# Kernel tuning notes

Measured on AMD Instinct MI355X. Metric: run time of the kernel, lower is better.

Reference implementation:

```python
import jax, jax.numpy as jnp
import numpy as np
from jax import lax

B, S, F, C = 64, 2048, 256, 32


def setup_inputs() -> dict:
    key = jax.random.key(0)
    ks = jax.random.split(key, 6)
    return {
        "X": jax.random.normal(ks[0], (B, S, F), dtype=jnp.float32),
        "W": jax.random.normal(ks[1], (C, F), dtype=jnp.float32) * (1.0 / np.sqrt(F)),
        "b": jax.random.normal(ks[2], (C,), dtype=jnp.float32) * 0.01,
        "transitions": jax.random.normal(ks[3], (C, C), dtype=jnp.float32) * 0.1,
        "start_transitions": jax.random.normal(ks[4], (C,), dtype=jnp.float32) * 0.1,
        "end_transitions": jax.random.normal(ks[5], (C,), dtype=jnp.float32) * 0.1,
    }


def reference(X, W, b, transitions, start_transitions, end_transitions):
    # Affine projection to emission scores: [B, S, C]
    emissions = jnp.einsum("bsf,cf->bsc", X, W) + b
    e = jnp.moveaxis(emissions, 1, 0)  # [S, B, C] for scan over time

    alpha0 = start_transitions[None, :] + e[0]  # [B, C]

    def viterbi_step(alpha, e_t):
        # scores[b, i, j] = alpha[b, i] + T[i, j] + e_t[b, j]
        scores = alpha[:, :, None] + transitions[None, :, :] + e_t[:, None, :]
        best = jnp.max(scores, axis=1)      # [B, C]
        bp = jnp.argmax(scores, axis=1)     # [B, C] backpointers
        return best, bp

    alpha_T, backptrs = lax.scan(viterbi_step, alpha0, e[1:])  # backptrs: [S-1, B, C]

    final = alpha_T + end_transitions[None, :]
    best_score = jnp.max(final, axis=-1)              # [B]
    last_tag = jnp.argmax(final, axis=-1)             # [B]

    def backtrack(tag, bp):
        prev = jnp.take_along_axis(bp, tag[:, None], axis=1)[:, 0]
        return prev, prev

    _, prev_tags = lax.scan(backtrack, last_tag, backptrs, reverse=True)  # [S-1, B]
    path = jnp.concatenate([prev_tags, last_tag[None, :]], axis=0)        # [S, B]
    return best_score, jnp.moveaxis(path, 0, 1)  # ([B], [B, S])
```

## Files before the change

### kernel.cpp

```cpp
#include <hip/hip_runtime.h>

#define BB 64
#define SS 2048
#define FF 256
#define CC 32
#define CH 64

typedef unsigned u32x2 __attribute__((ext_vector_type(2)));

__device__ __forceinline__ void plswap16(int a_in, int& x, int& y) {
#if __has_builtin(__builtin_amdgcn_permlane16_swap)
    u32x2 r = __builtin_amdgcn_permlane16_swap((unsigned)a_in, (unsigned)a_in, false, false);
    x = (int)r[0]; y = (int)r[1];
#else
    int xx = a_in, yy;
    asm volatile("v_mov_b32 %0, %1" : "=v"(yy) : "v"(a_in));
    asm volatile("v_permlane16_swap_b32 %0, %1" : "+v"(xx), "+v"(yy));
    x = xx; y = yy;
#endif
}
__device__ __forceinline__ void plswap32(int a_in, int& x, int& y) {
#if __has_builtin(__builtin_amdgcn_permlane32_swap)
    u32x2 r = __builtin_amdgcn_permlane32_swap((unsigned)a_in, (unsigned)a_in, false, false);
    x = (int)r[0]; y = (int)r[1];
#else
    int xx = a_in, yy;
    asm volatile("v_mov_b32 %0, %1" : "=v"(yy) : "v"(a_in));
    asm volatile("v_permlane32_swap_b32 %0, %1" : "+v"(xx), "+v"(yy));
    x = xx; y = yy;
#endif
}

#if __has_builtin(__builtin_amdgcn_mov_dpp)
#define ROT1(d, s, K) d = __builtin_amdgcn_mov_dpp(s, 0x120 + K, 0xF, 0xF, false)
#else
#define ROT1(d, s, K) d = __builtin_amdgcn_update_dpp(s, s, 0x120 + K, 0xF, 0xF, false)
#endif
#define ROTALL(arr, s) \
    arr[0] = s;        \
    ROT1(arr[1], s, 1);  ROT1(arr[2], s, 2);  ROT1(arr[3], s, 3);  \
    ROT1(arr[4], s, 4);  ROT1(arr[5], s, 5);  ROT1(arr[6], s, 6);  \
    ROT1(arr[7], s, 7);  ROT1(arr[8], s, 8);  ROT1(arr[9], s, 9);  \
    ROT1(arr[10], s, 10); ROT1(arr[11], s, 11); ROT1(arr[12], s, 12); \
    ROT1(arr[13], s, 13); ROT1(arr[14], s, 14); ROT1(arr[15], s, 15)

__device__ __forceinline__ float fmax3_(float a, float b, float c) { return fmaxf(fmaxf(a, b), c); }

__global__ __launch_bounds__(256) void emis_kernel(const float* __restrict__ X,
                                                   const float* __restrict__ W,
                                                   const float* __restrict__ bias,
                                                   float* __restrict__ em) {
    __shared__ __align__(16) float wsh[32 * 260];
    const int tid = threadIdx.x;
    const long rowbase = (long)blockIdx.x * 64;

    const float4* Wg = (const float4*)W;
#pragma unroll
    for (int i = 0; i < 8; ++i) {
        int idx = tid + i * 256;
        int r = idx >> 6, c4 = idx & 63;
        *(float4*)&wsh[r * 260 + c4 * 4] = Wg[idx];
    }
    __syncthreads();

    const int rp = tid >> 3;
    const int cgp = tid & 7;
    const long r0 = rowbase + 2 * rp, r1 = r0 + 1;
    const float4* X0 = (const float4*)(X + r0 * FF);
    const float4* X1 = (const float4*)(X + r1 * FF);

    float acc0[4] = {0.f, 0.f, 0.f, 0.f};
    float acc1[4] = {0.f, 0.f, 0.f, 0.f};

#pragma unroll 8
    for (int k4 = 0; k4 < 64; ++k4) {
        float4 xa = X0[k4];
        float4 xb = X1[k4];
#pragma unroll
        for (int jj = 0; jj < 4; ++jj) {
            float4 w = *(const float4*)&wsh[(cgp + 8 * jj) * 260 + k4 * 4];
            acc0[jj] = fmaf(xa.x, w.x, acc0[jj]);
            acc0[jj] = fmaf(xa.y, w.y, acc0[jj]);
            acc0[jj] = fmaf(xa.z, w.z, acc0[jj]);
            acc0[jj] = fmaf(xa.w, w.w, acc0[jj]);
            acc1[jj] = fmaf(xb.x, w.x, acc1[jj]);
            acc1[jj] = fmaf(xb.y, w.y, acc1[jj]);
            acc1[jj] = fmaf(xb.z, w.z, acc1[jj]);
            acc1[jj] = fmaf(xb.w, w.w, acc1[jj]);
        }
    }
#pragma unroll
    for (int jj = 0; jj < 4; ++jj) {
        int c = cgp + 8 * jj;
        float bj = bias[c];
        em[r0 * CC + c] = acc0[jj] + bj;
        em[r1 * CC + c] = acc1[jj] + bj;
    }
}

#define STEP2_ASM(avar, evar)                                                       \
    do {                                                                            \
        float x_, b_, q0_, q1_, q2_, q3_, q4_, q5_, q6_, q7_,                       \
              q8_, q9_, q10_, q11_, q12_, q13_, q14_, q15_;                         \
        asm volatile(                                                               \
            "v_mov_b32 %[x], %[aa]\n\t"                                             \
            "s_nop 1\n\t"                                                           \
            "v_permlane16_swap_b32 %[x], %[aa]\n\t"                                 \
            "s_nop 0\n\t"                                                           \
            "v_cndmask_b32 %[bb], %[aa], %[x], %[m16]\n\t"                          \
            "s_nop 1\n\t"                                                           \
            "v_add_f32 %[q0], %[bb], %[t0]\n\t"                                     \
            "v_add_f32_dpp %[q1], %[bb], %[t1] row_ror:1 row_mask:0xf bank_mask:0xf\n\t"  \
            "v_add_f32_dpp %[q2], %[bb], %[t2] row_ror:2 row_mask:0xf bank_mask:0xf\n\t"  \
            "v_add_f32_dpp %[q3], %[bb], %[t3] row_ror:3 row_mask:0xf bank_mask:0xf\n\t"  \
            "v_add_f32_dpp %[q4], %[bb], %[t4] row_ror:4 row_mask:0xf bank_mask:0xf\n\t"  \
            "v_add_f32_dpp %[q5], %[bb], %[t5] row_ror:5 row_mask:0xf bank_mask:0xf\n\t"  \
            "v_add_f32_dpp %[q6], %[bb], %[t6] row_ror:6 row_mask:0xf bank_mask:0xf\n\t"  \
            "v_add_f32_dpp %[q7], %[bb], %[t7] row_ror:7 row_mask:0xf bank_mask:0xf\n\t"  \
            "v_add_f32_dpp %[q8], %[bb], %[t8] row_ror:8 row_mask:0xf bank_mask:0xf\n\t"  \
            "v_add_f32_dpp %[q9], %[bb], %[t9] row_ror:9 row_mask:0xf bank_mask:0xf\n\t"  \
            "v_add_f32_dpp %[q10], %[bb], %[t10] row_ror:10 row_mask:0xf bank_mask:0xf\n\t" \
            "v_add_f32_dpp %[q11], %[bb], %[t11] row_ror:11 row_mask:0xf bank_mask:0xf\n\t" \
            "v_add_f32_dpp %[q12], %[bb], %[t12] row_ror:12 row_mask:0xf bank_mask:0xf\n\t" \
            "v_add_f32_dpp %[q13], %[bb], %[t13] row_ror:13 row_mask:0xf bank_mask:0xf\n\t" \
            "v_add_f32_dpp %[q14], %[bb], %[t14] row_ror:14 row_mask:0xf bank_mask:0xf\n\t" \
            "v_add_f32_dpp %[q15], %[bb], %[t15] row_ror:15 row_mask:0xf bank_mask:0xf\n\t" \
            "v_max3_f32 %[q0], %[q0], %[q1], %[q2]\n\t"                             \
            "v_max3_f32 %[q3], %[q3], %[q4], %[q5]\n\t"                             \
            "v_max3_f32 %[q6], %[q6], %[q7], %[q8]\n\t"                             \
            "v_max3_f32 %[q9], %[q9], %[q10], %[q11]\n\t"                           \
            "v_max3_f32 %[q12], %[q12], %[q13], %[q14]\n\t"                         \
            "v_max3_f32 %[q0], %[q0], %[q3], %[q6]\n\t"                             \
            "v_max3_f32 %[q9], %[q9], %[q12], %[q15]\n\t"                           \
            "v_max_f32 %[q0], %[q0], %[q9]\n\t"                                     \
            "v_mov_b32 %[x], %[q0]\n\t"                                             \
            "s_nop 1\n\t"                                                           \
            "v_permlane32_swap_b32 %[x], %[q0]\n\t"                                 \
            "s_nop 0\n\t"                                                           \
            "v_max_f32 %[q0], %[q0], %[x]\n\t"                                      \
            "v_add_f32 %[aa], %[q0], %[ee]\n\t"                                     \
            : [aa] "+v"(avar), [x] "=&v"(x_), [bb] "=&v"(b_),                       \
              [q0] "=&v"(q0_), [q1] "=&v"(q1_), [q2] "=&v"(q2_), [q3] "=&v"(q3_),   \
              [q4] "=&v"(q4_), [q5] "=&v"(q5_), [q6] "=&v"(q6_), [q7] "=&v"(q7_),   \
              [q8] "=&v"(q8_), [q9] "=&v"(q9_), [q10] "=&v"(q10_),                  \
              [q11] "=&v"(q11_), [q12] "=&v"(q12_), [q13] "=&v"(q13_),              \
              [q14] "=&v"(q14_), [q15] "=&v"(q15_)                                  \
            : [ee] "v"(evar), [t0] "v"(Ti[0]), [t1] "v"(Ti[1]), [t2] "v"(Ti[2]),    \
              [t3] "v"(Ti[3]), [t4] "v"(Ti[4]), [t5] "v"(Ti[5]), [t6] "v"(Ti[6]),   \
              [t7] "v"(Ti[7]), [t8] "v"(Ti[8]), [t9] "v"(Ti[9]), [t10] "v"(Ti[10]), \
              [t11] "v"(Ti[11]), [t12] "v"(Ti[12]), [t13] "v"(Ti[13]),              \
              [t14] "v"(Ti[14]), [t15] "v"(Ti[15]),                                 \
              [m16] "s"(mask16));                                                   \
    } while (0)

__global__ __launch_bounds__(64, 1) void viterbi_fwd4(float* __restrict__ em,
                                                      const float* __restrict__ T,
                                                      const float* __restrict__ startT,
                                                      const float* __restrict__ endT,
                                                      float* __restrict__ out) {
    const int l = threadIdx.x;
    const int b = blockIdx.x;
    const int j = l & 31;
    const int h = l >> 5;

    int p0, p1;
    plswap16(j, p0, p1);
    const bool c16 = (((p0 >> 4) & 1) == h);
    const int pm = c16 ? p0 : p1;
    int mk[16];
    ROTALL(mk, pm);

    const unsigned long long mask16 = __ballot(c16);

    float Ti[16];
#pragma unroll
    for (int k = 0; k < 16; ++k) Ti[k] = T[mk[k] * CC + j];

    float* eb = em + (long)b * SS * CC;

    float eq[8];
#pragma unroll
    for (int v = 0; v < 8; ++v) eq[v] = eb[v * 32 + j];

    float a = startT[j] + eq[0];
    eb[j] = a;
    eq[0] = eb[8 * 32 + j];

    int t = 1;
    for (int g = 0; g < 254; ++g) {
#pragma unroll
        for (int u = 0; u < 8; ++u) {
            STEP2_ASM(a, eq[t & 7]);
            eb[t * 32 + j] = a;
            eq[t & 7] = eb[(t + 8) * 32 + j];
            ++t;
        }
    }
#pragma unroll
    for (int u = 0; u < 7; ++u) {
        STEP2_ASM(a, eq[t & 7]);
        eb[t * 32 + j] = a;
        eq[t & 7] = eb[(t + 8) * 32 + j];
        ++t;
    }
#pragma unroll
    for (int u = 0; u < 8; ++u) {
        STEP2_ASM(a, eq[t & 7]);
        eb[t * 32 + j] = a;
        ++t;
    }

    float v = a + endT[j];
    int idx = j;
#pragma unroll
    for (int d = 1; d <= 16; d <<= 1) {
        float ovv = __shfl_xor(v, d);
        int   oii = __shfl_xor(idx, d);
        bool c = (ovv > v) || (ovv == v && oii < idx);
        v = c ? ovv : v;
        idx = c ? oii : idx;
    }
    if (l == 0) {
        out[b] = v;
        out[BB + (long)b * SS + (SS - 1)] = (float)idx;
    }
}

__global__ __launch_bounds__(64, 2) void bp_compose(const float* __restrict__ alpha,
                                                    const float* __restrict__ T,
                                                    unsigned* __restrict__ bp,
                                                    unsigned char* __restrict__ G) {
    const int l = threadIdx.x;
    const int j = l & 31;
    const int h = l >> 5;
    const int b = blockIdx.x >> 6;
    const int k = blockIdx.x & 63;

    int p0, p1;
    plswap16(j, p0, p1);
    const bool c16 = (((p0 >> 4) & 1) == h);
    const int pm = c16 ? p0 : p1;
    int mk[16];
    ROTALL(mk, pm);
    int q0p, q1p;
    plswap32(l, q0p, q1p);
    const bool pick0 = (q0p == (l ^ 32));

    float Ti[16];
    unsigned Bk[16];
#pragma unroll
    for (int kk = 0; kk < 16; ++kk) {
        Ti[kk] = T[mk[kk] * CC + j];
        Bk[kk] = 1u << mk[kk];
    }

    const float* A = alpha + (long)b * SS * CC;
    const int u0 = k << 5;

    float aq[8];
#pragma unroll
    for (int v = 0; v < 8; ++v) aq[v] = A[(u0 + v) * CC + j];

    unsigned sr[8];
#pragma unroll
    for (int p = 0; p < 8; ++p) sr[p] = 0u;

#pragma unroll
    for (int g8 = 0; g8 < 4; ++g8) {
#pragma unroll
        for (int v = 0; v < 8; ++v) {
            const int u = g8 * 8 + v;
            float av = aq[v];
            if (g8 < 3) aq[v] = A[(u0 + (g8 + 1) * 8 + v) * CC + j];

            int x, y;
            plswap16(__float_as_int(av), x, y);
            int base = c16 ? x : y;
            int rot[16];
            ROTALL(rot, base);
            float s[16];
#pragma unroll
            for (int kk = 0; kk < 16; ++kk) s[kk] = __int_as_float(rot[kk]) + Ti[kk];

            float m0 = fmax3_(s[0], s[1], s[2]);
            float m1 = fmax3_(s[3], s[4], s[5]);
            float m2 = fmax3_(s[6], s[7], s[8]);
            float m3 = fmax3_(s[9], s[10], s[11]);
            float m4 = fmax3_(s[12], s[13], s[14]);
            float mv = fmaxf(fmax3_(m0, m1, m2), fmax3_(m3, m4, s[15]));

            int xm, ym;
            plswap32(__float_as_int(mv), xm, ym);
            float ov = __int_as_float(pick0 ? xm : ym);
            float gv = fmaxf(mv, ov);

            unsigned c0 = (s[0] == gv) ? Bk[0] : 0u,   c1 = (s[1] == gv) ? Bk[1] : 0u;
            unsigned c2 = (s[2] == gv) ? Bk[2] : 0u,   c3 = (s[3] == gv) ? Bk[3] : 0u;
            unsigned c4 = (s[4] == gv) ? Bk[4] : 0u,   c5 = (s[5] == gv) ? Bk[5] : 0u;
            unsigned c6 = (s[6] == gv) ? Bk[6] : 0u,   c7 = (s[7] == gv) ? Bk[7] : 0u;
            unsigned c8 = (s[8] == gv) ? Bk[8] : 0u,   c9 = (s[9] == gv) ? Bk[9] : 0u;
            unsigned c10 = (s[10] == gv) ? Bk[10] : 0u, c11 = (s[11] == gv) ? Bk[11] : 0u;
            unsigned c12 = (s[12] == gv) ? Bk[12] : 0u, c13 = (s[13] == gv) ? Bk[13] : 0u;
            unsigned c14 = (s[14] == gv) ? Bk[14] : 0u, c15 = (s[15] == gv) ? Bk[15] : 0u;
            unsigned msk = ((c0 | c1 | c2) | (c3 | c4 | c5)) |
                           ((c6 | c7 | c8) | (c9 | c10 | c11)) |
                           ((c12 | c13 | c14) | c15);

            int xk, yk;
            plswap32((int)msk, xk, yk);
            unsigned om = (unsigned)(pick0 ? xk : yk);
            int wi = __builtin_ctz(msk | om);

            if (u == 31 && k == CH - 1) wi = j;
            sr[u >> 2] |= (unsigned)wi << ((u & 3) * 8);
        }
    }

#pragma unroll
    for (int p = 0; p < 8; ++p)
        bp[((unsigned)(8 * k + p) * BB + b) * CC + j] = sr[p];

    int g = j;
#pragma unroll
    for (int rel = 31; rel >= 0; --rel) {
        unsigned dw = (unsigned)__builtin_amdgcn_ds_bpermute((g | (l & 32)) << 2,
                                                             (int)sr[rel >> 2]);
        g = (int)((dw >> ((rel & 3) * 8)) & 31u);
    }
    G[(b * CH + k) * 32 + j] = (unsigned char)g;
}

__global__ __launch_bounds__(64) void bt_scan(const unsigned char* __restrict__ G,
                                              const float* __restrict__ out,
                                              int* __restrict__ tagB) {
    __shared__ unsigned char Gs[32 * CH * 32];
    const int l = threadIdx.x;
    const int bbase = blockIdx.x * 32;
    const float4* Gg = (const float4*)(G + (size_t)bbase * CH * 32);
    float4* Gls = (float4*)Gs;
#pragma unroll
    for (int i = 0; i < 64; ++i) Gls[l + i * 64] = Gg[l + i * 64];
    __syncthreads();

    if (l < 32) {
        const int b = bbase + l;
        int cur = (int)out[BB + (long)b * SS + (SS - 1)];
        for (int k = CH - 1; k >= 0; --k) {
            cur = Gs[(l * CH + k) * 32 + cur];
            tagB[b * CH + k] = cur;
        }
    }
}

__global__ __launch_bounds__(64, 4) void bt_emit(const unsigned* __restrict__ bp,
                                                 const int* __restrict__ tagB,
                                                 const float* __restrict__ outR,
                                                 float* __restrict__ out) {
    const int l = threadIdx.x;
    const int b = blockIdx.x >> 6;
    const int k = blockIdx.x & 63;

    unsigned sr[8];
#pragma unroll
    for (int p = 0; p < 8; ++p) sr[p] = bp[((unsigned)(8 * k + p) * BB + b) * CC + (l & 31)];

    int start = (k == CH - 1) ? (int)outR[BB + (long)b * SS + (SS - 1)]
                              : tagB[b * CH + k + 1];
    int g = start, cap = start;
#pragma unroll
    for (int rel = 31; rel >= 0; --rel) {
        unsigned dw = (unsigned)__builtin_amdgcn_ds_bpermute((g | (l & 32)) << 2,
                                                             (int)sr[rel >> 2]);
        g = (int)((dw >> ((rel & 3) * 8)) & 31u);
        cap = (l == rel) ? g : cap;
    }
    if (l < 32) out[BB + (long)b * SS + k * 32 + l] = (float)cap;
}

extern "C" void kernel_launch(void* const* d_in, const int* in_sizes, int n_in,
                              void* d_out, int out_size, void* d_ws, size_t ws_size,
                              hipStream_t stream) {
    const float* X      = (const float*)d_in[0];
    const float* W      = (const float*)d_in[1];
    const float* bias   = (const float*)d_in[2];
    const float* T      = (const float*)d_in[3];
    const float* startT = (const float*)d_in[4];
    const float* endT   = (const float*)d_in[5];
    float* out = (float*)d_out;

    float*    em = (float*)d_ws;
    unsigned* bp = (unsigned*)((char*)d_ws + (size_t)BB * SS * CC * 4);
    unsigned char* G    = (unsigned char*)d_ws + (20u << 20);
    int*           tagB = (int*)((char*)d_ws + (20u << 20) + 131072);

    emis_kernel<<<(BB * SS) / 64, 256, 0, stream>>>(X, W, bias, em);
    viterbi_fwd4<<<BB, 64, 0, stream>>>(em, T, startT, endT, out);
    bp_compose<<<BB * CH, 64, 0, stream>>>(em, T, bp, G);
    bt_scan<<<2, 64, 0, stream>>>(G, out, tagB);
    bt_emit<<<BB * CH, 64, 0, stream>>>(bp, tagB, out, out);
}
```

Measured before the change: 260.2 us.

## Fuse emission GEMM with Viterbi forward via per-batch progress counters

Merges the emission projection and the forward Viterbi recurrence into one launch. Emission blocks publish completion through per-batch atomic counters, and the forward wavefronts poll those counters so the serial recurrence can start while the remaining emissions are still being computed. Alpha values are now packed four timesteps per float4 store, and bp_compose reads them back in that matching packed layout. This relies on emission blocks being scheduled before the spinning forward blocks, and it adds a memset plus polling overhead.

```diff
diff --git a/kernel.cpp b/kernel.cpp
--- a/kernel.cpp
+++ b/kernel.cpp
@@ -45,58 +45,6 @@
     ROT1(arr[13], s, 13); ROT1(arr[14], s, 14); ROT1(arr[15], s, 15)
 
 __device__ __forceinline__ float fmax3_(float a, float b, float c) { return fmaxf(fmaxf(a, b), c); }
-
-__global__ __launch_bounds__(256) void emis_kernel(const float* __restrict__ X,
-                                                   const float* __restrict__ W,
-                                                   const float* __restrict__ bias,
-                                                   float* __restrict__ em) {
-    __shared__ __align__(16) float wsh[32 * 260];
-    const int tid = threadIdx.x;
-    const long rowbase = (long)blockIdx.x * 64;
-
-    const float4* Wg = (const float4*)W;
-#pragma unroll
-    for (int i = 0; i < 8; ++i) {
-        int idx = tid + i * 256;
-        int r = idx >> 6, c4 = idx & 63;
-        *(float4*)&wsh[r * 260 + c4 * 4] = Wg[idx];
-    }
-    __syncthreads();
-
-    const int rp = tid >> 3;
-    const int cgp = tid & 7;
-    const long r0 = rowbase + 2 * rp, r1 = r0 + 1;
-    const float4* X0 = (const float4*)(X + r0 * FF);
-    const float4* X1 = (const float4*)(X + r1 * FF);
-
-    float acc0[4] = {0.f, 0.f, 0.f, 0.f};
-    float acc1[4] = {0.f, 0.f, 0.f, 0.f};
-
-#pragma unroll 8
-    for (int k4 = 0; k4 < 64; ++k4) {
-        float4 xa = X0[k4];
-        float4 xb = X1[k4];
-#pragma unroll
-        for (int jj = 0; jj < 4; ++jj) {
-            float4 w = *(const float4*)&wsh[(cgp + 8 * jj) * 260 + k4 * 4];
-            acc0[jj] = fmaf(xa.x, w.x, acc0[jj]);
-            acc0[jj] = fmaf(xa.y, w.y, acc0[jj]);
-            acc0[jj] = fmaf(xa.z, w.z, acc0[jj]);
-            acc0[jj] = fmaf(xa.w, w.w, acc0[jj]);
-            acc1[jj] = fmaf(xb.x, w.x, acc1[jj]);
-            acc1[jj] = fmaf(xb.y, w.y, acc1[jj]);
-            acc1[jj] = fmaf(xb.z, w.z, acc1[jj]);
-            acc1[jj] = fmaf(xb.w, w.w, acc1[jj]);
-        }
-    }
-#pragma unroll
-    for (int jj = 0; jj < 4; ++jj) {
-        int c = cgp + 8 * jj;
-        float bj = bias[c];
-        em[r0 * CC + c] = acc0[jj] + bj;
-        em[r1 * CC + c] = acc1[jj] + bj;
-    }
-}
 
 #define STEP2_ASM(avar, evar)                                                       \
     do {                                                                            \
@@ -153,13 +101,76 @@
               [m16] "s"(mask16));                                                   \
     } while (0)
 
-__global__ __launch_bounds__(64, 1) void viterbi_fwd4(float* __restrict__ em,
+__global__ __launch_bounds__(256) void fused_emis_fwd(const float* __restrict__ X,
+                                                      const float* __restrict__ W,
+                                                      const float* __restrict__ bias,
                                                       const float* __restrict__ T,
                                                       const float* __restrict__ startT,
                                                       const float* __restrict__ endT,
-                                                      float* __restrict__ out) {
+                                                      float* __restrict__ em,
+                                                      float* __restrict__ out,
+                                                      int* __restrict__ prog) {
+    __shared__ __align__(16) float wsh[32 * 260];
+
+    if (blockIdx.x < 2048) {
+        const int tid = threadIdx.x;
+        const int g = blockIdx.x >> 6;
+        const int b = blockIdx.x & 63;
+        const long rowbase = (long)b * SS + (long)g * 64;
+
+        const float4* Wg = (const float4*)W;
+#pragma unroll
+        for (int i = 0; i < 8; ++i) {
+            int idx = tid + i * 256;
+            int r = idx >> 6, c4 = idx & 63;
+            *(float4*)&wsh[r * 260 + c4 * 4] = Wg[idx];
+        }
+        __syncthreads();
+
+        const int rp = tid >> 3;
+        const int cgp = tid & 7;
+        const long r0 = rowbase + 2 * rp, r1 = r0 + 1;
+        const float4* X0 = (const float4*)(X + r0 * FF);
+        const float4* X1 = (const float4*)(X + r1 * FF);
+
+        float acc0[4] = {0.f, 0.f, 0.f, 0.f};
+        float acc1[4] = {0.f, 0.f, 0.f, 0.f};
+
+#pragma unroll 8
+        for (int k4 = 0; k4 < 64; ++k4) {
+            float4 xa = X0[k4];
+            float4 xb = X1[k4];
+#pragma unroll
+            for (int jj = 0; jj < 4; ++jj) {
+                float4 w = *(const float4*)&wsh[(cgp + 8 * jj) * 260 + k4 * 4];
+                acc0[jj] = fmaf(xa.x, w.x, acc0[jj]);
+                acc0[jj] = fmaf(xa.y, w.y, acc0[jj]);
+                acc0[jj] = fmaf(xa.z, w.z, acc0[jj]);
+                acc0[jj] = fmaf(xa.w, w.w, acc0[jj]);
+                acc1[jj] = fmaf(xb.x, w.x, acc1[jj]);
+                acc1[jj] = fmaf(xb.y, w.y, acc1[jj]);
+                acc1[jj] = fmaf(xb.z, w.z, acc1[jj]);
+                acc1[jj] = fmaf(xb.w, w.w, acc1[jj]);
+            }
+        }
+#pragma unroll
+        for (int jj = 0; jj < 4; ++jj) {
+            int c = cgp + 8 * jj;
+            float bj = bias[c];
+            em[r0 * CC + c] = acc0[jj] + bj;
+            em[r1 * CC + c] = acc1[jj] + bj;
+        }
+
+        __syncthreads();
+        __threadfence();
+        if (tid == 0)
+            __hip_atomic_fetch_add(&prog[b], 1, __ATOMIC_RELEASE, __HIP_MEMORY_SCOPE_AGENT);
+        return;
+    }
+
+    if (threadIdx.x >= 64) return;
     const int l = threadIdx.x;
-    const int b = blockIdx.x;
+    const int b = blockIdx.x - 2048;
     const int j = l & 31;
     const int h = l >> 5;
 
@@ -176,39 +187,60 @@
 #pragma unroll
     for (int k = 0; k < 16; ++k) Ti[k] = T[mk[k] * CC + j];
 
+    int* pb = prog + b;
+    auto pollb = [&](int need) {
+        while (__hip_atomic_load(pb, __ATOMIC_ACQUIRE, __HIP_MEMORY_SCOPE_AGENT) < need)
+            __builtin_amdgcn_s_sleep(2);
+    };
+
     float* eb = em + (long)b * SS * CC;
+    float4* ev4 = (float4*)eb;
+
+    pollb(2);
 
     float eq[8];
 #pragma unroll
     for (int v = 0; v < 8; ++v) eq[v] = eb[v * 32 + j];
 
+    float4 av;
     float a = startT[j] + eq[0];
-    eb[j] = a;
+    av.x = a;
     eq[0] = eb[8 * 32 + j];
 
     int t = 1;
     for (int g = 0; g < 254; ++g) {
-#pragma unroll
-        for (int u = 0; u < 8; ++u) {
-            STEP2_ASM(a, eq[t & 7]);
-            eb[t * 32 + j] = a;
-            eq[t & 7] = eb[(t + 8) * 32 + j];
-            ++t;
-        }
-    }
-#pragma unroll
-    for (int u = 0; u < 7; ++u) {
-        STEP2_ASM(a, eq[t & 7]);
-        eb[t * 32 + j] = a;
-        eq[t & 7] = eb[(t + 8) * 32 + j];
-        ++t;
-    }
-#pragma unroll
-    for (int u = 0; u < 8; ++u) {
-        STEP2_ASM(a, eq[t & 7]);
-        eb[t * 32 + j] = a;
-        ++t;
-    }
+        if ((g & 7) == 0) {
+            int need = (g >> 3) + 2;
+            if (need > 32) need = 32;
+            pollb(need);
+        }
+        STEP2_ASM(a, eq[t & 7]); av.y = a; eq[t & 7] = eb[(t + 8) * 32 + j]; ++t;
+        STEP2_ASM(a, eq[t & 7]); av.z = a; eq[t & 7] = eb[(t + 8) * 32 + j]; ++t;
+        STEP2_ASM(a, eq[t & 7]); av.w = a; ev4[(t >> 2) * 32 + j] = av;
+        eq[t & 7] = eb[(t + 8) * 32 + j]; ++t;
+        STEP2_ASM(a, eq[t & 7]); av.x = a; eq[t & 7] = eb[(t + 8) * 32 + j]; ++t;
+        STEP2_ASM(a, eq[t & 7]); av.y = a; eq[t & 7] = eb[(t + 8) * 32 + j]; ++t;
+        STEP2_ASM(a, eq[t & 7]); av.z = a; eq[t & 7] = eb[(t + 8) * 32 + j]; ++t;
+        STEP2_ASM(a, eq[t & 7]); av.w = a; ev4[(t >> 2) * 32 + j] = av;
+        eq[t & 7] = eb[(t + 8) * 32 + j]; ++t;
+        STEP2_ASM(a, eq[t & 7]); av.x = a; eq[t & 7] = eb[(t + 8) * 32 + j]; ++t;
+    }
+    STEP2_ASM(a, eq[t & 7]); av.y = a; eq[t & 7] = eb[(t + 8) * 32 + j]; ++t;
+    STEP2_ASM(a, eq[t & 7]); av.z = a; eq[t & 7] = eb[(t + 8) * 32 + j]; ++t;
+    STEP2_ASM(a, eq[t & 7]); av.w = a; ev4[(t >> 2) * 32 + j] = av;
+    eq[t & 7] = eb[(t + 8) * 32 + j]; ++t;
+    STEP2_ASM(a, eq[t & 7]); av.x = a; eq[t & 7] = eb[(t + 8) * 32 + j]; ++t;
+    STEP2_ASM(a, eq[t & 7]); av.y = a; eq[t & 7] = eb[(t + 8) * 32 + j]; ++t;
+    STEP2_ASM(a, eq[t & 7]); av.z = a; eq[t & 7] = eb[(t + 8) * 32 + j]; ++t;
+    STEP2_ASM(a, eq[t & 7]); av.w = a; ev4[(t >> 2) * 32 + j] = av; ++t;
+    STEP2_ASM(a, eq[t & 7]); av.x = a; ++t;
+    STEP2_ASM(a, eq[t & 7]); av.y = a; ++t;
+    STEP2_ASM(a, eq[t & 7]); av.z = a; ++t;
+    STEP2_ASM(a, eq[t & 7]); av.w = a; ev4[(t >> 2) * 32 + j] = av; ++t;
+    STEP2_ASM(a, eq[t & 7]); av.x = a; ++t;
+    STEP2_ASM(a, eq[t & 7]); av.y = a; ++t;
+    STEP2_ASM(a, eq[t & 7]); av.z = a; ++t;
+    STEP2_ASM(a, eq[t & 7]); av.w = a; ev4[(t >> 2) * 32 + j] = av; ++t;
 
     float v = a + endT[j];
     int idx = j;
@@ -254,24 +286,22 @@
         Bk[kk] = 1u << mk[kk];
     }
 
-    const float* A = alpha + (long)b * SS * CC;
-    const int u0 = k << 5;
-
-    float aq[8];
-#pragma unroll
-    for (int v = 0; v < 8; ++v) aq[v] = A[(u0 + v) * CC + j];
+    const float4* A4 = (const float4*)(alpha + (long)b * SS * CC);
+    float4 aq4[8];
+#pragma unroll
+    for (int gg = 0; gg < 8; ++gg) aq4[gg] = A4[(8 * k + gg) * 32 + j];
 
     unsigned sr[8];
 #pragma unroll
     for (int p = 0; p < 8; ++p) sr[p] = 0u;
 
 #pragma unroll
-    for (int g8 = 0; g8 < 4; ++g8) {
-#pragma unroll
-        for (int v = 0; v < 8; ++v) {
-            const int u = g8 * 8 + v;
-            float av = aq[v];
-            if (g8 < 3) aq[v] = A[(u0 + (g8 + 1) * 8 + v) * CC + j];
+    for (int gg = 0; gg < 8; ++gg) {
+#pragma unroll
+        for (int v = 0; v < 4; ++v) {
+            const int u = gg * 4 + v;
+            float av = (v == 0) ? aq4[gg].x : (v == 1) ? aq4[gg].y
+                     : (v == 2) ? aq4[gg].z : aq4[gg].w;
 
             int x, y;
             plswap16(__float_as_int(av), x, y);
@@ -392,9 +422,10 @@
     unsigned* bp = (unsigned*)((char*)d_ws + (size_t)BB * SS * CC * 4);
     unsigned char* G    = (unsigned char*)d_ws + (20u << 20);
     int*           tagB = (int*)((char*)d_ws + (20u << 20) + 131072);
-
-    emis_kernel<<<(BB * SS) / 64, 256, 0, stream>>>(X, W, bias, em);
-    viterbi_fwd4<<<BB, 64, 0, stream>>>(em, T, startT, endT, out);
+    int*           prog = (int*)((char*)d_ws + (20u << 20) + 163840);
+
+    hipMemsetAsync(prog, 0, BB * sizeof(int), stream);
+    fused_emis_fwd<<<2048 + BB, 256, 0, stream>>>(X, W, bias, T, startT, endT, em, out, prog);
     bp_compose<<<BB * CH, 64, 0, stream>>>(em, T, bp, G);
     bt_scan<<<2, 64, 0, stream>>>(G, out, tagB);
     bt_emit<<<BB * CH, 64, 0, stream>>>(bp, tagB, out, out);
```

Result: slower. 555.4 us (+113.5%).
